# Kernel tuning notes

Measured on AMD Instinct MI355X. Metric: run time of the kernel, lower is better.

The kernel has to match this reference:

```python
import jax, jax.numpy as jnp
import numpy as np

BN_EPS = 1e-5


def _knn_idx(pos, k):
    # pos: (B, 3, N). Nearest-k by squared euclidean distance (self included).
    sq = jnp.sum(pos * pos, axis=1)                        # (B, N)
    inner = jnp.einsum('bcn,bcm->bnm', pos, pos)           # (B, N, N)
    neg_dist = 2.0 * inner - sq[:, :, None] - sq[:, None, :]
    _, idx = jax.lax.top_k(neg_dist, k)                    # (B, N, k)
    return idx


def setup_inputs() -> dict:
    key = jax.random.key(0)
    k1, k2, k3 = jax.random.split(key, 3)
    B, C, N, K, D = 4, 64, 8192, 16, 64
    return {
        'x': jax.random.normal(k1, (B, C, N), dtype=jnp.float32),
        'pos': jax.random.normal(k2, (B, 3, N), dtype=jnp.float32),
        'spectral_filter': jax.random.normal(k3, (K, C, D), dtype=jnp.float32),
        'gamma': jnp.ones((D,), dtype=jnp.float32),
        'beta': jnp.zeros((D,), dtype=jnp.float32),
    }


def reference(x, pos, spectral_filter, gamma, beta):
    k = spectral_filter.shape[0]
    idx = _knn_idx(pos, k)                                  # (B, N, k) int32
    # gather neighbors: nb[b, c, n, j] = x[b, c, idx[b, n, j]]
    nb = jax.vmap(lambda xf, ii: xf[:, ii])(x, idx)         # (B, C, N, k)
    edge = nb - x[:, :, :, None]                            # (B, C, N, k)
    # per-k small GEMM: 'bnkc,kcd->bnd' (channel dim is axis 1 here)
    out = jnp.einsum('bcnk,kcd->bnd', edge, spectral_filter)
    out = out.transpose(0, 2, 1)                            # (B, D, N)
    # BatchNorm1d, training mode (biased variance over batch and points)
    mean = jnp.mean(out, axis=(0, 2), keepdims=True)
    var = jnp.var(out, axis=(0, 2), keepdims=True)
    out = (out - mean) * jax.lax.rsqrt(var + BN_EPS)
    return out * gamma[None, :, None] + beta[None, :, None]
```

## Files before the change

### kernel.cpp

```cpp
#include <hip/hip_runtime.h>
#include <hip/hip_bf16.h>

#define NPTS 8192
#define NQ   32768
#define KNN  16
#define SCAP 112

#define OFF_XT   0
#define OFF_FBIG (8*1024*1024)
#define OFF_SUMS (OFF_FBIG + 278528)
#define OFF_IDX  (OFF_SUMS + 512)
#define OFF_PRE  (OFF_IDX + 2*1024*1024)
#define OFF_SQ   OFF_PRE

__device__ __forceinline__ float sq3(float x, float y, float z) {
    #pragma clang fp contract(off)
    float xx = x * x;
    float yy = y * y;
    float zz = z * z;
    return (xx + yy) + zz;
}
__device__ __forceinline__ float negd2(float qx, float qy, float qz, float sqn,
                                       float mx, float my, float mz, float sqm) {
    #pragma clang fp contract(off)
    float p0 = qx * mx;
    float inn = __builtin_fmaf(qz, mz, __builtin_fmaf(qy, my, p0));
    float t = 2.0f * inn;
    float u = t - sqn;
    return u - sqm;
}
#define KEY_EPS2 2.0e-3f

__device__ __forceinline__ float rfl(float v) {
    return __uint_as_float(__builtin_amdgcn_readfirstlane(__float_as_uint(v)));
}

__global__ __launch_bounds__(256) void k_prep(const float* __restrict__ x,
                                              const float* __restrict__ F,
                                              const float* __restrict__ pos,
                                              float* __restrict__ xT,
                                              float* __restrict__ Fb,
                                              float* __restrict__ sums,
                                              float* __restrict__ sqa) {
    int bid = blockIdx.x;
    if (bid < 512) {
        __shared__ float tile[64][65];
        int lane = threadIdx.x & 63, wid = threadIdx.x >> 6;
        int b = bid >> 7, nt = bid & 127;
        int n0 = nt * 64;
        for (int rr = 0; rr < 16; ++rr) {
            int c = wid * 16 + rr;
            tile[c][lane] = x[((size_t)b * 64 + c) * NPTS + n0 + lane];
        }
        __syncthreads();
        for (int rr = 0; rr < 16; ++rr) {
            int r = wid * 16 + rr;
            xT[((size_t)(b * NPTS + n0 + r)) * 64 + lane] = tile[lane][r];
        }
    } else if (bid < 528) {
        int j = bid - 512;
        for (int e = threadIdx.x; e < 4096; e += 256)
            Fb[j * 4096 + e] = F[j * 4096 + e];
    } else if (bid == 528) {
        for (int e = threadIdx.x; e < 4096; e += 256) {
            float s = 0.f;
            for (int k = 0; k < 16; ++k) s += F[k * 4096 + e];
            Fb[16 * 4096 + e] = -s;
        }
    } else if (bid == 529) {
        if (threadIdx.x < 128) sums[threadIdx.x] = 0.f;
    } else {
        int g = (bid - 530) * 256 + threadIdx.x;
        int b = g >> 13, n = g & (NPTS - 1);
        const float* pb = pos + (size_t)b * 3 * NPTS;
        sqa[g] = sq3(pb[n], pb[NPTS + n], pb[2 * NPTS + n]);
    }
}

__device__ __forceinline__ void sel16(const float* lm, float* thr) {
    unsigned up[4], pfx[4];
    #pragma unroll
    for (int i = 0; i < 4; ++i) {
        unsigned s = __float_as_uint(lm[i]);
        up[i]  = s ^ ((unsigned)((int)s >> 31) | 0x80000000u);
        pfx[i] = 0u;
    }
    for (int bit = 31; bit >= 0; --bit) {
        unsigned bmask = 1u << bit;
        #pragma unroll
        for (int i = 0; i < 4; ++i) {
            unsigned trial = pfx[i] | bmask;
            unsigned long long m = __ballot(up[i] >= trial);
            if (__popcll(m) >= 16) pfx[i] = trial;
        }
    }
    #pragma unroll
    for (int i = 0; i < 4; ++i) {
        unsigned p = pfx[i];
        unsigned sbits = (p & 0x80000000u) ? (p ^ 0x80000000u) : ~p;
        thr[i] = __uint_as_float(sbits) - KEY_EPS2;
    }
}

__global__ __launch_bounds__(256, 4) void k_knn(const float* __restrict__ pos,
                                                const float* __restrict__ sqa,
                                                int* __restrict__ idxo) {
    __shared__ int   cnt[16];
    __shared__ int   outI[16][16];
    __shared__ float thrs[16];
    __shared__ union {
        float lm[16][256];
        struct {
            unsigned short sidx[16][SCAP];
            float          skey[16][SCAP];
        } ab;
    } sh;
    int t = threadIdx.x, lane = t & 63, wid = t >> 6;
    int qblk = blockIdx.x * 16;
    int b = qblk >> 13;
    const float* px = pos + (size_t)b * 3 * NPTS;
    const float* py = px + NPTS;
    const float* pz = py + NPTS;
    const float* sb = sqa + (size_t)b * NPTS;
    int qn = qblk & (NPTS - 1);

    float tqx[16], tqy[16], tqz[16];
    #pragma unroll
    for (int i = 0; i < 16; ++i) {
        tqx[i] = rfl(2.0f * px[qn + i]);
        tqy[i] = rfl(2.0f * py[qn + i]);
        tqz[i] = rfl(2.0f * pz[qn + i]);
    }
    if (lane < 4) cnt[wid * 4 + lane] = 0;
    if (lane < 16) {
        #pragma unroll
        for (int i = 0; i < 4; ++i) outI[wid * 4 + i][lane] = qn + wid * 4 + i;
    }

    float lm[16];
    #pragma unroll
    for (int i = 0; i < 16; ++i) lm[i] = -3.4e38f;
    int base = wid * 2048;
    for (int it = 0; it < 8; ++it) {
        int m = base + it * 256 + lane * 4;
        float4 X = *(const float4*)(px + m);
        float4 Y = *(const float4*)(py + m);
        float4 Z = *(const float4*)(pz + m);
        float4 S = *(const float4*)(sb + m);
        #pragma unroll
        for (int i = 0; i < 16; ++i) {
            float a0 = __builtin_fmaf(tqx[i], X.x, __builtin_fmaf(tqy[i], Y.x, __builtin_fmaf(tqz[i], Z.x, -S.x)));
            float a1 = __builtin_fmaf(tqx[i], X.y, __builtin_fmaf(tqy[i], Y.y, __builtin_fmaf(tqz[i], Z.y, -S.y)));
            float a2 = __builtin_fmaf(tqx[i], X.z, __builtin_fmaf(tqy[i], Y.z, __builtin_fmaf(tqz[i], Z.z, -S.z)));
            float a3 = __builtin_fmaf(tqx[i], X.w, __builtin_fmaf(tqy[i], Y.w, __builtin_fmaf(tqz[i], Z.w, -S.w)));
            float m012 = fmaxf(fmaxf(a0, a1), a2);
            lm[i] = fmaxf(fmaxf(m012, a3), lm[i]);
        }
    }
    #pragma unroll
    for (int i = 0; i < 16; ++i) sh.lm[i][wid * 64 + lane] = lm[i];
    __syncthreads();

    {
        float comb[4];
        #pragma unroll
        for (int j = 0; j < 4; ++j) {
            int i = wid * 4 + j;
            float c0 = sh.lm[i][lane];
            float c1 = sh.lm[i][64 + lane];
            float c2 = sh.lm[i][128 + lane];
            float c3 = sh.lm[i][192 + lane];
            comb[j] = fmaxf(fmaxf(c0, c1), fmaxf(c2, c3));
        }
        float thr4[4];
        sel16(comb, thr4);
        if (lane == 0) {
            #pragma unroll
            for (int j = 0; j < 4; ++j) thrs[wid * 4 + j] = thr4[j];
        }
    }
    __syncthreads();
    float thr[16];
    #pragma unroll
    for (int i = 0; i < 16; ++i) thr[i] = rfl(thrs[i]);

    for (int it = 0; it < 8; ++it) {
        int m = base + it * 256 + lane * 4;
        float4 X = *(const float4*)(px + m);
        float4 Y = *(const float4*)(py + m);
        float4 Z = *(const float4*)(pz + m);
        float4 S = *(const float4*)(sb + m);
        #pragma unroll
        for (int i = 0; i < 16; ++i) {
            float a0 = __builtin_fmaf(tqx[i], X.x, __builtin_fmaf(tqy[i], Y.x, __builtin_fmaf(tqz[i], Z.x, -S.x)));
            float a1 = __builtin_fmaf(tqx[i], X.y, __builtin_fmaf(tqy[i], Y.y, __builtin_fmaf(tqz[i], Z.y, -S.y)));
            float a2 = __builtin_fmaf(tqx[i], X.z, __builtin_fmaf(tqy[i], Y.z, __builtin_fmaf(tqz[i], Z.z, -S.z)));
            float a3 = __builtin_fmaf(tqx[i], X.w, __builtin_fmaf(tqy[i], Y.w, __builtin_fmaf(tqz[i], Z.w, -S.w)));
            if (a0 >= thr[i]) { int s_ = atomicAdd(&cnt[i],1); if (s_<SCAP) sh.ab.sidx[i][s_] = (unsigned short)m; }
            if (a1 >= thr[i]) { int s_ = atomicAdd(&cnt[i],1); if (s_<SCAP) sh.ab.sidx[i][s_] = (unsigned short)(m+1); }
            if (a2 >= thr[i]) { int s_ = atomicAdd(&cnt[i],1); if (s_<SCAP) sh.ab.sidx[i][s_] = (unsigned short)(m+2); }
            if (a3 >= thr[i]) { int s_ = atomicAdd(&cnt[i],1); if (s_<SCAP) sh.ab.sidx[i][s_] = (unsigned short)(m+3); }
        }
    }
    __syncthreads();

    #pragma unroll 1
    for (int i = 0; i < 4; ++i) {
        int lq = wid * 4 + i;
        float qxx = px[qn + lq], qyy = py[qn + lq], qzz = pz[qn + lq];
        float sqn = sb[qn + lq];
        int S = cnt[lq]; if (S > SCAP) S = SCAP;
        for (int p = lane; p < S; p += 64) {
            int m = sh.ab.sidx[lq][p];
            sh.ab.skey[lq][p] = negd2(qxx, qyy, qzz, sqn,
                                      px[m], py[m], pz[m], sb[m]);
        }
    }
    __syncthreads();

    #pragma unroll 1
    for (int i = 0; i < 4; ++i) {
        int lq = wid * 4 + i;
        int S = cnt[lq]; if (S > SCAP) S = SCAP;
        for (int p = lane; p < S; p += 64) {
            int m = sh.ab.sidx[lq][p];
            float km = sh.ab.skey[lq][p];
            int rank = 0;
            for (int j = 0; j < S; ++j) {
                float kj = sh.ab.skey[lq][j];
                int ij = sh.ab.sidx[lq][j];
                if (kj > km || (kj == km && ij < m)) rank++;
            }
            if (rank < KNN) outI[lq][rank] = m;
        }
    }
    __syncthreads();
    {
        int lq = t >> 4;
        idxo[(size_t)(qblk + lq) * KNN + (t & 15)] = outI[lq][t & 15];
    }
}

#define CPAD 68
__global__ __launch_bounds__(256) void k_conv(const float* __restrict__ xT,
                                              const float* __restrict__ Fb,
                                              const int* __restrict__ idx,
                                              float* __restrict__ outp,
                                              float* __restrict__ sums) {
    __shared__ float At[64][CPAD];
    __shared__ float Bt[64 * 64];
    int t = threadIdx.x;
    int q0 = blockIdx.x * 64;
    int bbase = q0 & ~(NPTS - 1);
    int qi0 = (t >> 4) * 4;
    int dj0 = (t & 15) * 4;
    int r = t & 63;
    int s = t >> 6;

    float acc[4][4];
    #pragma unroll
    for (int a = 0; a < 4; ++a)
        #pragma unroll
        for (int bb = 0; bb < 4; ++bb) acc[a][bb] = 0.f;

    float4 ga0, ga1, ga2, ga3;
    float4 gb0, gb1, gb2, gb3;

    #define LOADJ(J)                                                           \
    {                                                                          \
        int qg = q0 + r;                                                       \
        int nbr = ((J) < 16) ? (idx[(size_t)qg * KNN + (J)] & (NPTS - 1))      \
                             : (qg & (NPTS - 1));                              \
        const float* src = xT + ((size_t)(bbase + nbr) * 64 + s * 16);         \
        ga0 = *(const float4*)(src);                                           \
        ga1 = *(const float4*)(src + 4);                                       \
        ga2 = *(const float4*)(src + 8);                                       \
        ga3 = *(const float4*)(src + 12);                                      \
        const float* fj = Fb + (J) * 4096;                                     \
        gb0 = *(const float4*)(fj +    0 + t * 4);                             \
        gb1 = *(const float4*)(fj + 1024 + t * 4);                            \
        gb2 = *(const float4*)(fj + 2048 + t * 4);                            \
        gb3 = *(const float4*)(fj + 3072 + t * 4);                            \
    }

    LOADJ(0);
    for (int j = 0; j < 17; ++j) {
        __syncthreads();
        {
            int c0 = s * 16;
            At[c0+ 0][r] = ga0.x; At[c0+ 1][r] = ga0.y; At[c0+ 2][r] = ga0.z; At[c0+ 3][r] = ga0.w;
            At[c0+ 4][r] = ga1.x; At[c0+ 5][r] = ga1.y; At[c0+ 6][r] = ga1.z; At[c0+ 7][r] = ga1.w;
            At[c0+ 8][r] = ga2.x; At[c0+ 9][r] = ga2.y; At[c0+10][r] = ga2.z; At[c0+11][r] = ga2.w;
            At[c0+12][r] = ga3.x; At[c0+13][r] = ga3.y; At[c0+14][r] = ga3.z; At[c0+15][r] = ga3.w;
            *(float4*)&Bt[   0 + t * 4] = gb0;
            *(float4*)&Bt[1024 + t * 4] = gb1;
            *(float4*)&Bt[2048 + t * 4] = gb2;
            *(float4*)&Bt[3072 + t * 4] = gb3;
        }
        __syncthreads();
        if (j < 16) LOADJ(j + 1);
        #pragma unroll 8
        for (int k = 0; k < 64; ++k) {
            float4 av = *(const float4*)&At[k][qi0];
            float4 bv = *(const float4*)&Bt[k * 64 + dj0];
            acc[0][0] = fmaf(av.x, bv.x, acc[0][0]);
            acc[0][1] = fmaf(av.x, bv.y, acc[0][1]);
            acc[0][2] = fmaf(av.x, bv.z, acc[0][2]);
            acc[0][3] = fmaf(av.x, bv.w, acc[0][3]);
            acc[1][0] = fmaf(av.y, bv.x, acc[1][0]);
            acc[1][1] = fmaf(av.y, bv.y, acc[1][1]);
            acc[1][2] = fmaf(av.y, bv.z, acc[1][2]);
            acc[1][3] = fmaf(av.y, bv.w, acc[1][3]);
            acc[2][0] = fmaf(av.z, bv.x, acc[2][0]);
            acc[2][1] = fmaf(av.z, bv.y, acc[2][1]);
            acc[2][2] = fmaf(av.z, bv.z, acc[2][2]);
            acc[2][3] = fmaf(av.z, bv.w, acc[2][3]);
            acc[3][0] = fmaf(av.w, bv.x, acc[3][0]);
            acc[3][1] = fmaf(av.w, bv.y, acc[3][1]);
            acc[3][2] = fmaf(av.w, bv.z, acc[3][2]);
            acc[3][3] = fmaf(av.w, bv.w, acc[3][3]);
        }
    }
    #undef LOADJ
    #pragma unroll
    for (int qi = 0; qi < 4; ++qi) {
        float4 o = make_float4(acc[qi][0], acc[qi][1], acc[qi][2], acc[qi][3]);
        *(float4*)(outp + (size_t)(q0 + qi0 + qi) * 64 + dj0) = o;
    }
    {
        __syncthreads();
        float* P  = Bt;
        float* P2 = Bt + 1024;
        int g = t >> 4;
        #pragma unroll
        for (int dd = 0; dd < 4; ++dd) {
            float sv = ((acc[0][dd] + acc[1][dd]) + acc[2][dd]) + acc[3][dd];
            float qv = fmaf(acc[3][dd], acc[3][dd],
                       fmaf(acc[2][dd], acc[2][dd],
                       fmaf(acc[1][dd], acc[1][dd], acc[0][dd] * acc[0][dd])));
            P [g * 64 + dj0 + dd] = sv;
            P2[g * 64 + dj0 + dd] = qv;
        }
        __syncthreads();
        if (t < 64) {
            float a = 0.f, b2 = 0.f;
            #pragma unroll
            for (int gg = 0; gg < 16; ++gg) {
                a  += P [gg * 64 + t];
                b2 += P2[gg * 64 + t];
            }
            atomicAdd(&sums[t], a);
            atomicAdd(&sums[64 + t], b2);
        }
    }
}

__global__ __launch_bounds__(256) void k_bn(const float* __restrict__ outp,
                                            const float* __restrict__ sums,
                                            const float* __restrict__ gamma,
                                            const float* __restrict__ beta,
                                            float* __restrict__ out) {
    __shared__ float tile[64][65];
    __shared__ float sa[64], sb[64];
    int lane = threadIdx.x & 63, wid = threadIdx.x >> 6;
    int b = blockIdx.x >> 7, nt = blockIdx.x & 127;
    int n0 = nt * 64;
    if (threadIdx.x < 64) {
        const float inv = 1.f / 32768.f;
        float mean = sums[threadIdx.x] * inv;
        float var = sums[64 + threadIdx.x] * inv - mean * mean;
        float rs = rsqrtf(var + 1e-5f);
        float a = rs * gamma[threadIdx.x];
        sa[threadIdx.x] = a;
        sb[threadIdx.x] = beta[threadIdx.x] - mean * a;
    }
    for (int rr = 0; rr < 16; ++rr) {
        int r = wid * 16 + rr;
        tile[r][lane] = outp[((size_t)(b * NPTS + n0 + r)) * 64 + lane];
    }
    __syncthreads();
    for (int rr = 0; rr < 16; ++rr) {
        int dr = wid * 16 + rr;
        out[((size_t)b * 64 + dr) * NPTS + n0 + lane] =
            fmaf(tile[lane][dr], sa[dr], sb[dr]);
    }
}

extern "C" void kernel_launch(void* const* d_in, const int* in_sizes, int n_in,
                              void* d_out, int out_size, void* d_ws, size_t ws_size,
                              hipStream_t stream) {
    (void)in_sizes; (void)n_in; (void)out_size; (void)ws_size;
    const float* x     = (const float*)d_in[0];
    const float* pos   = (const float*)d_in[1];
    const float* F     = (const float*)d_in[2];
    const float* gamma = (const float*)d_in[3];
    const float* beta  = (const float*)d_in[4];
    float* out = (float*)d_out;

    char* ws = (char*)d_ws;
    float* xT   = (float*)(ws + OFF_XT);
    float* Fb   = (float*)(ws + OFF_FBIG);
    float* sums = (float*)(ws + OFF_SUMS);
    int*   idx  = (int*)(ws + OFF_IDX);
    float* pre  = (float*)(ws + OFF_PRE);
    float* sqa  = (float*)(ws + OFF_SQ);

    k_prep<<<658, 256, 0, stream>>>(x, F, pos, xT, Fb, sums, sqa);
    k_knn<<<2048, 256, 0, stream>>>(pos, sqa, idx);
    k_conv<<<512, 256, 0, stream>>>(xT, Fb, idx, pre, sums);
    k_bn<<<512, 256, 0, stream>>>(pre, sums, gamma, beta, out);
}
```

Baseline: 259.8 us.

## Fuse batchnorm into conv kernel via cooperative grid sync

Launches the conv kernel cooperatively, waits on a grid-wide barrier once the BN sums are accumulated, then normalizes the register accumulators and writes the final transposed output directly. This removes the intermediate pre-BN buffer write and read along with the separate BN kernel launch. In exchange it adds a grid barrier, needs all 512 blocks to be co-resident, and writes the output as strided float4 stores along N.

```diff
diff --git a/kernel.cpp b/kernel.cpp
--- a/kernel.cpp
+++ b/kernel.cpp
@@ -1,5 +1,6 @@
 #include <hip/hip_runtime.h>
 #include <hip/hip_bf16.h>
+#include <hip/hip_cooperative_groups.h>
 
 #define NPTS 8192
 #define NQ   32768
@@ -245,8 +246,10 @@
 __global__ __launch_bounds__(256) void k_conv(const float* __restrict__ xT,
                                               const float* __restrict__ Fb,
                                               const int* __restrict__ idx,
-                                              float* __restrict__ outp,
-                                              float* __restrict__ sums) {
+                                              const float* __restrict__ gamma,
+                                              const float* __restrict__ beta,
+                                              float* __restrict__ sums,
+                                              float* __restrict__ out) {
     __shared__ float At[64][CPAD];
     __shared__ float Bt[64 * 64];
     int t = threadIdx.x;
@@ -322,11 +325,6 @@
         }
     }
     #undef LOADJ
-    #pragma unroll
-    for (int qi = 0; qi < 4; ++qi) {
-        float4 o = make_float4(acc[qi][0], acc[qi][1], acc[qi][2], acc[qi][3]);
-        *(float4*)(outp + (size_t)(q0 + qi0 + qi) * 64 + dj0) = o;
-    }
     {
         __syncthreads();
         float* P  = Bt;
@@ -353,36 +351,25 @@
             atomicAdd(&sums[64 + t], b2);
         }
     }
-}
-
-__global__ __launch_bounds__(256) void k_bn(const float* __restrict__ outp,
-                                            const float* __restrict__ sums,
-                                            const float* __restrict__ gamma,
-                                            const float* __restrict__ beta,
-                                            float* __restrict__ out) {
-    __shared__ float tile[64][65];
-    __shared__ float sa[64], sb[64];
-    int lane = threadIdx.x & 63, wid = threadIdx.x >> 6;
-    int b = blockIdx.x >> 7, nt = blockIdx.x & 127;
-    int n0 = nt * 64;
-    if (threadIdx.x < 64) {
+    cooperative_groups::this_grid().sync();
+    {
         const float inv = 1.f / 32768.f;
-        float mean = sums[threadIdx.x] * inv;
-        float var = sums[64 + threadIdx.x] * inv - mean * mean;
-        float rs = rsqrtf(var + 1e-5f);
-        float a = rs * gamma[threadIdx.x];
-        sa[threadIdx.x] = a;
-        sb[threadIdx.x] = beta[threadIdx.x] - mean * a;
-    }
-    for (int rr = 0; rr < 16; ++rr) {
-        int r = wid * 16 + rr;
-        tile[r][lane] = outp[((size_t)(b * NPTS + n0 + r)) * 64 + lane];
-    }
-    __syncthreads();
-    for (int rr = 0; rr < 16; ++rr) {
-        int dr = wid * 16 + rr;
-        out[((size_t)b * 64 + dr) * NPTS + n0 + lane] =
-            fmaf(tile[lane][dr], sa[dr], sb[dr]);
+        int bb = q0 >> 13;
+        int qpos = (q0 & (NPTS - 1)) + qi0;
+        #pragma unroll
+        for (int dd = 0; dd < 4; ++dd) {
+            int d = dj0 + dd;
+            float mean = sums[d] * inv;
+            float var  = sums[64 + d] * inv - mean * mean;
+            float rs = rsqrtf(var + 1e-5f);
+            float a = rs * gamma[d];
+            float sh_ = beta[d] - mean * a;
+            float4 o = make_float4(fmaf(acc[0][dd], a, sh_),
+                                   fmaf(acc[1][dd], a, sh_),
+                                   fmaf(acc[2][dd], a, sh_),
+                                   fmaf(acc[3][dd], a, sh_));
+            *(float4*)(out + ((size_t)bb * 64 + d) * NPTS + qpos) = o;
+        }
     }
 }
 
@@ -402,11 +389,14 @@
     float* Fb   = (float*)(ws + OFF_FBIG);
     float* sums = (float*)(ws + OFF_SUMS);
     int*   idx  = (int*)(ws + OFF_IDX);
-    float* pre  = (float*)(ws + OFF_PRE);
     float* sqa  = (float*)(ws + OFF_SQ);
 
     k_prep<<<658, 256, 0, stream>>>(x, F, pos, xT, Fb, sums, sqa);
     k_knn<<<2048, 256, 0, stream>>>(pos, sqa, idx);
-    k_conv<<<512, 256, 0, stream>>>(xT, Fb, idx, pre, sums);
-    k_bn<<<512, 256, 0, stream>>>(pre, sums, gamma, beta, out);
-}
+    {
+        void* args[] = { (void*)&xT, (void*)&Fb, (void*)&idx,
+                         (void*)&gamma, (void*)&beta, (void*)&sums, (void*)&out };
+        (void)hipLaunchCooperativeKernel((const void*)k_conv, dim3(512), dim3(256),
+                                         args, 0, stream);
+    }
+}
```

New measurement: 299.7 us. 1.15x slower.
